# Kernel tuning notes

Measured on AMD Instinct MI355X. Metric: run time of the kernel, lower is better.

The kernel has to match this reference:

```python
import jax, jax.numpy as jnp
import numpy as np
import math

N_NODES = 100000
N_EDGES = 1600000
IN_DIM = 32
OUT_DIM = 32

def setup_inputs() -> dict:
    key = jax.random.key(0)
    k1, k2, k3, k4 = jax.random.split(key, 4)
    X = jax.random.normal(k1, (N_NODES, IN_DIM), dtype=jnp.float32)
    src_idx = jax.random.randint(k2, (N_EDGES,), 0, N_NODES, dtype=jnp.int64)
    dst_idx = jax.random.randint(k3, (N_EDGES,), 0, N_NODES, dtype=jnp.int64)
    # weights init: uniform(-stdv, stdv), stdv = 1/sqrt(output_dim)
    stdv = 1.0 / math.sqrt(OUT_DIM)
    W = jax.random.uniform(k4, (IN_DIM, OUT_DIM), dtype=jnp.float32,
                           minval=-stdv, maxval=stdv)
    return {"X": X, "W": W, "src_idx": src_idx, "dst_idx": dst_idx}

def reference(X, W, src_idx, dst_idx):
    # GIN sum-aggregation SpMM: agg[i] = sum_{j in N(i)} X[j]
    agg = jax.ops.segment_sum(X[src_idx], dst_idx, num_segments=N_NODES)
    # dense GEMM: X_prime = agg @ W
    return agg @ W
```

## Files before the change

### kernel.cpp

```cpp
#include <hip/hip_runtime.h>

#define N_DIM 32
#define NPB 64
#define NB_FINE_MAX 2048
#define CAPFINE 1280
#define CEPB 4096
#define FT 512
#define GROWS 512

__device__ __forceinline__ unsigned f2bf_rne(float f) {
    unsigned u = __float_as_uint(f);
    return (u + 0x7FFFu + ((u >> 16) & 1u)) >> 16;
}
__device__ __forceinline__ float bf2f(unsigned h) {
    return __uint_as_float(h << 16);
}

__global__ __launch_bounds__(FT) void k_fused(const float* __restrict__ X,
                                              const float* __restrict__ W,
                                              unsigned* __restrict__ Y,
                                              const int* __restrict__ src,
                                              const int* __restrict__ dst,
                                              int* __restrict__ cursorF0,
                                              int* __restrict__ pairs,
                                              int n_nodes, int n_edges,
                                              int nb_fine, int nblk_g) {
    __shared__ float Wlds[N_DIM * N_DIM];
    __shared__ int h[NB_FINE_MAX];
    __shared__ int gb[NB_FINE_MAX];
    const int t = threadIdx.x;

    if (blockIdx.x < nblk_g) {
        for (int i = t; i < N_DIM * N_DIM; i += FT) Wlds[i] = W[i];
        __syncthreads();
        const int r = blockIdx.x * GROWS + t;
        if (r >= n_nodes) return;

        float x[N_DIM];
        const float4* xr = (const float4*)(X + (size_t)r * N_DIM);
#pragma unroll
        for (int i = 0; i < N_DIM / 4; ++i) {
            float4 v = xr[i];
            x[4 * i + 0] = v.x; x[4 * i + 1] = v.y;
            x[4 * i + 2] = v.z; x[4 * i + 3] = v.w;
        }
        float acc[N_DIM];
#pragma unroll
        for (int c = 0; c < N_DIM; ++c) acc[c] = 0.0f;
#pragma unroll
        for (int k = 0; k < N_DIM; ++k) {
            const float xk = x[k];
#pragma unroll
            for (int c = 0; c < N_DIM; ++c)
                acc[c] = fmaf(xk, Wlds[k * N_DIM + c], acc[c]);
        }
        unsigned yp[16];
#pragma unroll
        for (int q = 0; q < 16; ++q)
            yp[q] = f2bf_rne(acc[2 * q]) | (f2bf_rne(acc[2 * q + 1]) << 16);
        uint4* yr = (uint4*)(Y + (size_t)r * 16);
#pragma unroll
        for (int i = 0; i < 4; ++i)
            yr[i] = make_uint4(yp[4 * i], yp[4 * i + 1],
                               yp[4 * i + 2], yp[4 * i + 3]);
    } else {
        for (int i = t; i < nb_fine; i += FT) h[i] = 0;
        __syncthreads();
        const int start = (blockIdx.x - nblk_g) * CEPB;

        int vw[CEPB / FT], cw[CEPB / FT], rw[CEPB / FT];
#pragma unroll
        for (int k = 0; k < CEPB / FT; ++k) {
            int e = start + t + k * FT;
            if (e < n_edges) {
                int d = dst[e];
                int c = d >> 6;
                cw[k] = c;
                vw[k] = src[e] | ((d & 63) << 17);
                rw[k] = atomicAdd(&h[c], 1);
            } else {
                cw[k] = -1;
            }
        }
        __syncthreads();
        for (int i = t; i < nb_fine; i += FT) {
            int c = h[i];
            gb[i] = c ? atomicAdd(&cursorF0[i], c) : 0;
        }
        __syncthreads();
#pragma unroll
        for (int k = 0; k < CEPB / FT; ++k)
            if (cw[k] >= 0) {
                int idx = gb[cw[k]] + rw[k];
                if (idx < CAPFINE)
                    pairs[(size_t)cw[k] * CAPFINE + idx] = vw[k];
            }
    }
}

__device__ __forceinline__ void addv(float* acc, uint4 v) {
    acc[0] += bf2f(v.x & 0xFFFFu); acc[1] += bf2f(v.x >> 16);
    acc[2] += bf2f(v.y & 0xFFFFu); acc[3] += bf2f(v.y >> 16);
    acc[4] += bf2f(v.z & 0xFFFFu); acc[5] += bf2f(v.z >> 16);
    acc[6] += bf2f(v.w & 0xFFFFu); acc[7] += bf2f(v.w >> 16);
}

__global__ __launch_bounds__(256) void k_agg(const uint4* __restrict__ Y4,
                                             const int* __restrict__ cursorF0,
                                             const int* __restrict__ pairs,
                                             float* __restrict__ out,
                                             int n_nodes) {
    __shared__ int sbin[CAPFINE];
    __shared__ int cnt[NPB];
    __shared__ int cst[NPB];
    __shared__ int excl[NPB];

    const int t = threadIdx.x;
    const int b = blockIdx.x;
    const int len = min(cursorF0[b], CAPFINE);
    const size_t segbase = (size_t)b * CAPFINE;
    const int g = t >> 2;
    const int l = t & 3;

    if (t < NPB) cnt[t] = 0;
    __syncthreads();

    int pv[CAPFINE / 256], rv[CAPFINE / 256];
#pragma unroll
    for (int k = 0; k < CAPFINE / 256; ++k) {
        int i = t + k * 256;
        if (i < len) {
            int p = pairs[segbase + i];
            pv[k] = p;
            rv[k] = atomicAdd(&cnt[p >> 17], 1);
        } else {
            pv[k] = -1;
        }
    }
    __syncthreads();
    if (t < 64) {
        int c0 = cnt[t];
        int c = c0;
#pragma unroll
        for (int off = 1; off < 64; off <<= 1) {
            int u = __shfl_up(c, off, 64);
            if (t >= off) c += u;
        }
        cst[t] = c;
        excl[t] = c - c0;
    }
    __syncthreads();
#pragma unroll
    for (int k = 0; k < CAPFINE / 256; ++k) {
        if (pv[k] >= 0) {
            int p = pv[k];
            sbin[excl[p >> 17] + rv[k]] = p & 0x1FFFF;
        }
    }
    __syncthreads();

    float acc[8];
#pragma unroll
    for (int i = 0; i < 8; ++i) acc[i] = 0.0f;

    const int s1 = cst[g];
    const int s0 = s1 - cnt[g];
    for (int e = s0; e < s1; e += 4) {
        const int m = s1 - e;
        int i0 = sbin[e];
        int i1 = sbin[e + ((m > 1) ? 1 : 0)];
        int i2 = sbin[e + ((m > 2) ? 2 : 0)];
        int i3 = sbin[e + ((m > 3) ? 3 : 0)];
        uint4 v0 = Y4[(size_t)i0 * 4 + l];
        uint4 v1 = Y4[(size_t)i1 * 4 + l];
        uint4 v2 = Y4[(size_t)i2 * 4 + l];
        uint4 v3 = Y4[(size_t)i3 * 4 + l];
        addv(acc, v0);
        if (m > 1) addv(acc, v1);
        if (m > 2) addv(acc, v2);
        if (m > 3) addv(acc, v3);
    }

    const int node = b * NPB + g;
    if (node < n_nodes) {
        ((float4*)out)[(size_t)node * 8 + 2 * l] =
            make_float4(acc[0], acc[1], acc[2], acc[3]);
        ((float4*)out)[(size_t)node * 8 + 2 * l + 1] =
            make_float4(acc[4], acc[5], acc[6], acc[7]);
    }
}

extern "C" void kernel_launch(void* const* d_in, const int* in_sizes, int n_in,
                              void* d_out, int out_size, void* d_ws, size_t ws_size,
                              hipStream_t stream) {
    const float* X   = (const float*)d_in[0];
    const float* W   = (const float*)d_in[1];
    const int*   src = (const int*)d_in[2];
    const int*   dst = (const int*)d_in[3];
    float* out = (float*)d_out;

    const int n_nodes = in_sizes[0] / N_DIM;
    const int n_edges = in_sizes[2];
    const int nb = (n_nodes + NPB - 1) / NPB;

    unsigned* Y   = (unsigned*)d_ws;
    int* cursorF0 = (int*)(Y + (size_t)n_nodes * 16);
    int* pairs    = cursorF0 + NB_FINE_MAX;

    const int nblk_g = (n_nodes + GROWS - 1) / GROWS;
    const int nblk_c = (n_edges + CEPB - 1) / CEPB;

    hipMemsetAsync(cursorF0, 0, (size_t)NB_FINE_MAX * sizeof(int), stream);

    k_fused<<<nblk_g + nblk_c, FT, 0, stream>>>(X, W, Y, src, dst, cursorF0, pairs,
                                                n_nodes, n_edges, nb, nblk_g);
    k_agg<<<nb, 256, 0, stream>>>((const uint4*)Y, cursorF0, pairs, out, n_nodes);
}
```

Baseline: 123.2 us.

## Replace global-atomic bucketing with per-segment bins merged in aggregation kernel

The edge-bucketing blocks now each handle a larger edge segment and write into private per-segment, per-bin slots capped at CAPB entries, with no global atomics. They also emit per-segment counts, which removes the memset and the global cursor atomics. The aggregation kernel prefix-sums the per-segment counts for its bin and gathers the pairs from all segments into shared memory before its existing local sort and accumulate. The cost is a strided gather across up to 98 segments per bin in k_agg, fewer bucketing blocks, and possibly dropped edges if a bin gets more than 48 hits within one segment.

```diff
diff --git a/kernel.cpp b/kernel.cpp
--- a/kernel.cpp
+++ b/kernel.cpp
@@ -4,7 +4,9 @@
 #define NPB 64
 #define NB_FINE_MAX 2048
 #define CAPFINE 1280
-#define CEPB 4096
+#define CAPB 48
+#define CEPB 16384
+#define NSEG_MAX 128
 #define FT 512
 #define GROWS 512
 
@@ -21,13 +23,12 @@
                                               unsigned* __restrict__ Y,
                                               const int* __restrict__ src,
                                               const int* __restrict__ dst,
-                                              int* __restrict__ cursorF0,
-                                              int* __restrict__ pairs,
+                                              int* __restrict__ cnt2,
+                                              int* __restrict__ pairs2,
                                               int n_nodes, int n_edges,
-                                              int nb_fine, int nblk_g) {
+                                              int nbins, int nblk_g) {
     __shared__ float Wlds[N_DIM * N_DIM];
     __shared__ int h[NB_FINE_MAX];
-    __shared__ int gb[NB_FINE_MAX];
     const int t = threadIdx.x;
 
     if (blockIdx.x < nblk_g) {
@@ -64,37 +65,34 @@
             yr[i] = make_uint4(yp[4 * i], yp[4 * i + 1],
                                yp[4 * i + 2], yp[4 * i + 3]);
     } else {
-        for (int i = t; i < nb_fine; i += FT) h[i] = 0;
+        for (int i = t; i < NB_FINE_MAX; i += FT) h[i] = 0;
         __syncthreads();
-        const int start = (blockIdx.x - nblk_g) * CEPB;
-
-        int vw[CEPB / FT], cw[CEPB / FT], rw[CEPB / FT];
-#pragma unroll
-        for (int k = 0; k < CEPB / FT; ++k) {
-            int e = start + t + k * FT;
-            if (e < n_edges) {
-                int d = dst[e];
-                int c = d >> 6;
-                cw[k] = c;
-                vw[k] = src[e] | ((d & 63) << 17);
-                rw[k] = atomicAdd(&h[c], 1);
-            } else {
-                cw[k] = -1;
+        const int seg = blockIdx.x - nblk_g;
+        const int start = seg * CEPB;
+        int* __restrict__ myseg = pairs2 + (size_t)seg * nbins * CAPB;
+
+        for (int kb = 0; kb < CEPB / FT / 8; ++kb) {
+            int vw[8], cw[8], rw[8];
+#pragma unroll
+            for (int k = 0; k < 8; ++k) {
+                int e = start + t + (kb * 8 + k) * FT;
+                if (e < n_edges) {
+                    int d = dst[e];
+                    cw[k] = d >> 6;
+                    vw[k] = src[e] | ((d & 63) << 17);
+                    rw[k] = atomicAdd(&h[cw[k]], 1);
+                } else {
+                    cw[k] = -1;
+                }
             }
+#pragma unroll
+            for (int k = 0; k < 8; ++k)
+                if (cw[k] >= 0 && rw[k] < CAPB)
+                    myseg[cw[k] * CAPB + rw[k]] = vw[k];
         }
         __syncthreads();
-        for (int i = t; i < nb_fine; i += FT) {
-            int c = h[i];
-            gb[i] = c ? atomicAdd(&cursorF0[i], c) : 0;
-        }
-        __syncthreads();
-#pragma unroll
-        for (int k = 0; k < CEPB / FT; ++k)
-            if (cw[k] >= 0) {
-                int idx = gb[cw[k]] + rw[k];
-                if (idx < CAPFINE)
-                    pairs[(size_t)cw[k] * CAPFINE + idx] = vw[k];
-            }
+        for (int i = t; i < nbins; i += FT)
+            cnt2[(size_t)seg * nbins + i] = min(h[i], CAPB);
     }
 }
 
@@ -106,22 +104,62 @@
 }
 
 __global__ __launch_bounds__(256) void k_agg(const uint4* __restrict__ Y4,
-                                             const int* __restrict__ cursorF0,
-                                             const int* __restrict__ pairs,
+                                             const int* __restrict__ cnt2,
+                                             const int* __restrict__ pairs2,
                                              float* __restrict__ out,
-                                             int n_nodes) {
+                                             int n_nodes, int nbins, int nseg) {
+    __shared__ int qbuf[CAPFINE];
     __shared__ int sbin[CAPFINE];
+    __shared__ int scnt[NSEG_MAX];
+    __shared__ int soff[NSEG_MAX];
+    __shared__ int slen;
     __shared__ int cnt[NPB];
     __shared__ int cst[NPB];
     __shared__ int excl[NPB];
 
     const int t = threadIdx.x;
     const int b = blockIdx.x;
-    const int len = min(cursorF0[b], CAPFINE);
-    const size_t segbase = (size_t)b * CAPFINE;
-    const int g = t >> 2;
-    const int l = t & 3;
-
+
+    for (int i = t; i < NSEG_MAX; i += 256)
+        scnt[i] = (i < nseg) ? cnt2[(size_t)i * nbins + b] : 0;
+    __syncthreads();
+
+    if (t < 64) {
+        int a = scnt[t];
+        int x = a;
+#pragma unroll
+        for (int o = 1; o < 64; o <<= 1) {
+            int u = __shfl_up(x, o, 64);
+            if (t >= o) x += u;
+        }
+        int b2 = scnt[64 + t];
+        int y = b2;
+#pragma unroll
+        for (int o = 1; o < 64; o <<= 1) {
+            int u = __shfl_up(y, o, 64);
+            if (t >= o) y += u;
+        }
+        int tot1 = __shfl(x, 63, 64);
+        int tot2 = __shfl(y, 63, 64);
+        soff[t] = x - a;
+        soff[64 + t] = tot1 + y - b2;
+        if (t == 0) slen = tot1 + tot2;
+    }
+    __syncthreads();
+    const int len = min(slen, CAPFINE);
+
+    {
+        const int w = t >> 6;
+        const int lane = t & 63;
+        for (int s = w; s < nseg; s += 4) {
+            int c = scnt[s];
+            if (lane < c) {
+                int p = pairs2[((size_t)s * nbins + b) * CAPB + lane];
+                int idx = soff[s] + lane;
+                if (idx < CAPFINE) qbuf[idx] = p;
+            }
+        }
+    }
     if (t < NPB) cnt[t] = 0;
     __syncthreads();
 
@@ -130,9 +168,9 @@
     for (int k = 0; k < CAPFINE / 256; ++k) {
         int i = t + k * 256;
         if (i < len) {
-            int p = pairs[segbase + i];
+            int p = qbuf[i];
             pv[k] = p;
-            rv[k] = atomicAdd(&cnt[p >> 17], 1);
+            rv[k] = atomicAdd(&cnt[(p >> 17) & 63], 1);
         } else {
             pv[k] = -1;
         }
@@ -154,11 +192,13 @@
     for (int k = 0; k < CAPFINE / 256; ++k) {
         if (pv[k] >= 0) {
             int p = pv[k];
-            sbin[excl[p >> 17] + rv[k]] = p & 0x1FFFF;
-        }
-    }
-    __syncthreads();
-
+            sbin[excl[(p >> 17) & 63] + rv[k]] = p & 0x1FFFF;
+        }
+    }
+    __syncthreads();
+
+    const int g = t >> 2;
+    const int l = t & 3;
     float acc[8];
 #pragma unroll
     for (int i = 0; i < 8; ++i) acc[i] = 0.0f;
@@ -201,18 +241,17 @@
 
     const int n_nodes = in_sizes[0] / N_DIM;
     const int n_edges = in_sizes[2];
-    const int nb = (n_nodes + NPB - 1) / NPB;
-
-    unsigned* Y   = (unsigned*)d_ws;
-    int* cursorF0 = (int*)(Y + (size_t)n_nodes * 16);
-    int* pairs    = cursorF0 + NB_FINE_MAX;
+    const int nbins = (n_nodes + NPB - 1) / NPB;
+    const int nseg  = (n_edges + CEPB - 1) / CEPB;
+
+    unsigned* Y  = (unsigned*)d_ws;
+    int* cnt2    = (int*)(Y + (size_t)n_nodes * 16);
+    int* pairs2  = cnt2 + (size_t)nseg * nbins;
 
     const int nblk_g = (n_nodes + GROWS - 1) / GROWS;
-    const int nblk_c = (n_edges + CEPB - 1) / CEPB;
-
-    hipMemsetAsync(cursorF0, 0, (size_t)NB_FINE_MAX * sizeof(int), stream);
-
-    k_fused<<<nblk_g + nblk_c, FT, 0, stream>>>(X, W, Y, src, dst, cursorF0, pairs,
-                                                n_nodes, n_edges, nb, nblk_g);
-    k_agg<<<nb, 256, 0, stream>>>((const uint4*)Y, cursorF0, pairs, out, n_nodes);
-}
+
+    k_fused<<<nblk_g + nseg, FT, 0, stream>>>(X, W, Y, src, dst, cnt2, pairs2,
+                                              n_nodes, n_edges, nbins, nblk_g);
+    k_agg<<<nbins, 256, 0, stream>>>((const uint4*)Y, cnt2, pairs2, out,
+                                     n_nodes, nbins, nseg);
+}
```

Result: slower. 132.6 us (+7.7%).

## Replace global atomic bin cursors with per-segment histogram, scan, and scatter passes

Applied to the files above, without the earlier changes.

Splits edge binning into three passes: a per-segment histogram written to a count matrix, a column-wise scan giving each segment's offset in each bin, and a scatter kernel that writes pairs using those offsets. This removes global atomicAdd contention on the bin cursors and the memset, and makes bin placement deterministic. In exchange it adds two kernel launches, rereads dst, and the scan kernel makes strided reads over a ~391x1563 count matrix.

```diff
diff --git a/kernel.cpp b/kernel.cpp
--- a/kernel.cpp
+++ b/kernel.cpp
@@ -19,15 +19,12 @@
 __global__ __launch_bounds__(FT) void k_fused(const float* __restrict__ X,
                                               const float* __restrict__ W,
                                               unsigned* __restrict__ Y,
-                                              const int* __restrict__ src,
                                               const int* __restrict__ dst,
-                                              int* __restrict__ cursorF0,
-                                              int* __restrict__ pairs,
+                                              int* __restrict__ cnt2,
                                               int n_nodes, int n_edges,
-                                              int nb_fine, int nblk_g) {
+                                              int nbins, int nblk_g) {
     __shared__ float Wlds[N_DIM * N_DIM];
     __shared__ int h[NB_FINE_MAX];
-    __shared__ int gb[NB_FINE_MAX];
     const int t = threadIdx.x;
 
     if (blockIdx.x < nblk_g) {
@@ -64,38 +61,79 @@
             yr[i] = make_uint4(yp[4 * i], yp[4 * i + 1],
                                yp[4 * i + 2], yp[4 * i + 3]);
     } else {
-        for (int i = t; i < nb_fine; i += FT) h[i] = 0;
+        for (int i = t; i < nbins; i += FT) h[i] = 0;
         __syncthreads();
-        const int start = (blockIdx.x - nblk_g) * CEPB;
-
-        int vw[CEPB / FT], cw[CEPB / FT], rw[CEPB / FT];
+        const int seg = blockIdx.x - nblk_g;
+        const int start = seg * CEPB;
 #pragma unroll
         for (int k = 0; k < CEPB / FT; ++k) {
             int e = start + t + k * FT;
-            if (e < n_edges) {
-                int d = dst[e];
-                int c = d >> 6;
-                cw[k] = c;
-                vw[k] = src[e] | ((d & 63) << 17);
-                rw[k] = atomicAdd(&h[c], 1);
-            } else {
-                cw[k] = -1;
-            }
+            if (e < n_edges) atomicAdd(&h[dst[e] >> 6], 1);
         }
         __syncthreads();
-        for (int i = t; i < nb_fine; i += FT) {
-            int c = h[i];
-            gb[i] = c ? atomicAdd(&cursorF0[i], c) : 0;
-        }
-        __syncthreads();
-#pragma unroll
-        for (int k = 0; k < CEPB / FT; ++k)
-            if (cw[k] >= 0) {
-                int idx = gb[cw[k]] + rw[k];
-                if (idx < CAPFINE)
-                    pairs[(size_t)cw[k] * CAPFINE + idx] = vw[k];
-            }
-    }
+        for (int i = t; i < nbins; i += FT)
+            cnt2[(size_t)seg * nbins + i] = h[i];
+    }
+}
+
+__global__ __launch_bounds__(64) void k_scan(int* __restrict__ cnt2,
+                                             int* __restrict__ binlen,
+                                             int nbins, int nseg) {
+    const int b = blockIdx.x;
+    const int t = threadIdx.x;
+    int run = 0;
+    for (int ch = 0; ch * 64 < nseg; ++ch) {
+        const int s = ch * 64 + t;
+        int a = (s < nseg) ? cnt2[(size_t)s * nbins + b] : 0;
+        int x = a;
+#pragma unroll
+        for (int o = 1; o < 64; o <<= 1) {
+            int u = __shfl_up(x, o, 64);
+            if (t >= o) x += u;
+        }
+        if (s < nseg) cnt2[(size_t)s * nbins + b] = run + x - a;
+        run += __shfl(x, 63, 64);
+    }
+    if (t == 0) binlen[b] = min(run, CAPFINE);
+}
+
+__global__ __launch_bounds__(FT) void k_scat(const int* __restrict__ src,
+                                             const int* __restrict__ dst,
+                                             const int* __restrict__ offs2,
+                                             int* __restrict__ pairs,
+                                             int n_edges, int nbins) {
+    __shared__ int h[NB_FINE_MAX];
+    __shared__ int gb[NB_FINE_MAX];
+    const int t = threadIdx.x;
+    const int seg = blockIdx.x;
+    const int start = seg * CEPB;
+
+    for (int i = t; i < nbins; i += FT) {
+        h[i] = 0;
+        gb[i] = offs2[(size_t)seg * nbins + i];
+    }
+    __syncthreads();
+
+    int vw[CEPB / FT], cw[CEPB / FT], rw[CEPB / FT];
+#pragma unroll
+    for (int k = 0; k < CEPB / FT; ++k) {
+        int e = start + t + k * FT;
+        if (e < n_edges) {
+            int d = dst[e];
+            cw[k] = d >> 6;
+            vw[k] = src[e] | ((d & 63) << 17);
+            rw[k] = atomicAdd(&h[cw[k]], 1);
+        } else {
+            cw[k] = -1;
+        }
+    }
+#pragma unroll
+    for (int k = 0; k < CEPB / FT; ++k)
+        if (cw[k] >= 0) {
+            int idx = gb[cw[k]] + rw[k];
+            if (idx < CAPFINE)
+                pairs[(size_t)cw[k] * CAPFINE + idx] = vw[k];
+        }
 }
 
 __device__ __forceinline__ void addv(float* acc, uint4 v) {
@@ -106,7 +144,7 @@
 }
 
 __global__ __launch_bounds__(256) void k_agg(const uint4* __restrict__ Y4,
-                                             const int* __restrict__ cursorF0,
+                                             const int* __restrict__ binlen,
                                              const int* __restrict__ pairs,
                                              float* __restrict__ out,
                                              int n_nodes) {
@@ -117,7 +155,7 @@
 
     const int t = threadIdx.x;
     const int b = blockIdx.x;
-    const int len = min(cursorF0[b], CAPFINE);
+    const int len = binlen[b];
     const size_t segbase = (size_t)b * CAPFINE;
     const int g = t >> 2;
     const int l = t & 3;
@@ -201,18 +239,19 @@
 
     const int n_nodes = in_sizes[0] / N_DIM;
     const int n_edges = in_sizes[2];
-    const int nb = (n_nodes + NPB - 1) / NPB;
-
-    unsigned* Y   = (unsigned*)d_ws;
-    int* cursorF0 = (int*)(Y + (size_t)n_nodes * 16);
-    int* pairs    = cursorF0 + NB_FINE_MAX;
+    const int nbins = (n_nodes + NPB - 1) / NPB;
+    const int nseg  = (n_edges + CEPB - 1) / CEPB;
+
+    unsigned* Y  = (unsigned*)d_ws;
+    int* cnt2    = (int*)(Y + (size_t)n_nodes * 16);
+    int* binlen  = cnt2 + (size_t)nseg * nbins;
+    int* pairs   = binlen + NB_FINE_MAX;
 
     const int nblk_g = (n_nodes + GROWS - 1) / GROWS;
-    const int nblk_c = (n_edges + CEPB - 1) / CEPB;
-
-    hipMemsetAsync(cursorF0, 0, (size_t)NB_FINE_MAX * sizeof(int), stream);
-
-    k_fused<<<nblk_g + nblk_c, FT, 0, stream>>>(X, W, Y, src, dst, cursorF0, pairs,
-                                                n_nodes, n_edges, nb, nblk_g);
-    k_agg<<<nb, 256, 0, stream>>>((const uint4*)Y, cursorF0, pairs, out, n_nodes);
-}
+
+    k_fused<<<nblk_g + nseg, FT, 0, stream>>>(X, W, Y, dst, cnt2,
+                                              n_nodes, n_edges, nbins, nblk_g);
+    k_scan<<<nbins, 64, 0, stream>>>(cnt2, binlen, nbins, nseg);
+    k_scat<<<nseg, FT, 0, stream>>>(src, dst, cnt2, pairs, n_edges, nbins);
+    k_agg<<<nbins, 256, 0, stream>>>((const uint4*)Y, binlen, pairs, out, n_nodes);
+}
```

Result: slower. 139.3 us (+13.1%).
